# Kernel optimization log

Measured on AMD Instinct MI355X. Metric: run time of the kernel, lower is better.

The kernel has to match this reference:

```python
import jax, jax.numpy as jnp
from jax import lax
import numpy as np

C, C_MID, K_ENC, K_UP, SCALE = 128, 64, 3, 5, 2
B, H, W = 4, 48, 48
BN_EPS = 1e-3  # ultralytics Conv BN eps
EPS = 1e-6


def setup_inputs() -> dict:
    key = jax.random.key(0)
    ks = jax.random.split(key, 12)
    n_enc = (SCALE * K_UP) ** 2  # 100
    return {
        "x": jax.random.uniform(ks[0], (B, C, H, W), dtype=jnp.float32),
        "comp_w": jax.random.normal(ks[1], (C_MID, C, 1, 1), dtype=jnp.float32) * 0.05,
        "comp_bn_g": jax.random.normal(ks[2], (C_MID,), dtype=jnp.float32) * 0.1 + 1.0,
        "comp_bn_b": jax.random.normal(ks[3], (C_MID,), dtype=jnp.float32) * 0.1,
        "comp_bn_m": jax.random.normal(ks[4], (C_MID,), dtype=jnp.float32) * 0.1,
        "comp_bn_v": jax.random.uniform(ks[5], (C_MID,), dtype=jnp.float32, minval=0.5, maxval=1.5),
        "enc_w": jax.random.normal(ks[6], (n_enc, C_MID, K_ENC, K_ENC), dtype=jnp.float32) * 0.05,
        "enc_bn_g": jax.random.normal(ks[7], (n_enc,), dtype=jnp.float32) * 0.1 + 1.0,
        "enc_bn_b": jax.random.normal(ks[8], (n_enc,), dtype=jnp.float32) * 0.1,
        "enc_bn_m": jax.random.normal(ks[9], (n_enc,), dtype=jnp.float32) * 0.1,
        "enc_bn_v": jax.random.uniform(ks[10], (n_enc,), dtype=jnp.float32, minval=0.5, maxval=1.5),
    }


def _conv_bn(x, w, g, b, m, v, pad, act):
    y = lax.conv_general_dilated(
        x, w, window_strides=(1, 1), padding=[(pad, pad), (pad, pad)],
        dimension_numbers=("NCHW", "OIHW", "NCHW"))
    scale = (g * lax.rsqrt(v + BN_EPS))[None, :, None, None]
    y = (y - m[None, :, None, None]) * scale + b[None, :, None, None]
    if act:  # SiLU
        y = y * jax.nn.sigmoid(y)
    return y


def reference(x, comp_w, comp_bn_g, comp_bn_b, comp_bn_m, comp_bn_v,
              enc_w, enc_bn_g, enc_bn_b, enc_bn_m, enc_bn_v):
    b, c, h, w = x.shape
    h_, w_ = h * SCALE, w * SCALE

    # ---- SAGamma: self-adaptive gamma correction ----
    gray = 0.299 * x[:, 0] + 0.587 * x[:, 1] + 0.114 * x[:, 2]  # (b,h,w)
    gm = jnp.mean(gray, axis=(1, 2), keepdims=True)              # (b,1,1)
    gs = jnp.std(gray, axis=(1, 2), ddof=1, keepdims=True)       # unbiased, like torch
    gamma = 0.8 + (1.2 - 0.8) * gm / (gm + jnp.maximum(gs, EPS))
    gamma = jnp.clip(gamma, 0.8, 1.2)[:, None]                   # (b,1,1,1)
    x = jnp.power(x + EPS, gamma)

    # ---- CARAFE ----
    # kernel prediction: comp (1x1 Conv+BN+SiLU) -> enc (3x3 Conv+BN, no act)
    Wk = _conv_bn(x, comp_w, comp_bn_g, comp_bn_b, comp_bn_m, comp_bn_v, pad=0, act=True)
    Wk = _conv_bn(Wk, enc_w, enc_bn_g, enc_bn_b, enc_bn_m, enc_bn_v, pad=K_ENC // 2, act=False)
    # pixel shuffle: (b, 25*s*s, h, w) -> (b, 25, h_, w_)
    k2 = K_UP * K_UP
    Wk = Wk.reshape(b, k2, SCALE, SCALE, h, w)
    Wk = Wk.transpose(0, 1, 4, 2, 5, 3).reshape(b, k2, h_, w_)
    Wk = jax.nn.softmax(Wk, axis=1)

    # nearest upsample x2
    Xu = jnp.repeat(jnp.repeat(x, SCALE, axis=2), SCALE, axis=3)  # (b,c,h_,w_)
    # unfold with kernel 5, dilation 2, pad 4 -> (b,c,25,h_,w_), torch (c,kh,kw) ordering
    pad = (K_UP // 2) * SCALE
    Xp = jnp.pad(Xu, ((0, 0), (0, 0), (pad, pad), (pad, pad)))
    patches = jnp.stack(
        [Xp[:, :, i * SCALE:i * SCALE + h_, j * SCALE:j * SCALE + w_]
         for i in range(K_UP) for j in range(K_UP)], axis=2)      # (b,c,25,h_,w_)

    return jnp.einsum("bkhw,bckhw->bchw", Wk, patches)
```

## Files before the change

### kernel.cpp

```cpp
#include <hip/hip_runtime.h>
#include <hip/hip_bf16.h>
#include <math.h>

#define CB   128
#define CMID 64
#define NENC 100
#define HH   48
#define WW   48
#define BB   4
#define HW   (HH*WW)
#define H2   (HH*2)
#define W2   (WW*2)
#define PS   56
#define PROWS 50
#define PCOL0 4
#define PLANE (PROWS*PS)
#define EG   2

__global__ void halo_kernel(float* __restrict__ y1p) {
    int idx = blockIdx.x * blockDim.x + threadIdx.x;
    int plane = idx / 124;
    int t = idx % 124;
    float* p = y1p + (size_t)plane * PLANE;
    float4 z = make_float4(0.f, 0.f, 0.f, 0.f);
    if (t < 14) {
        *(float4*)(p + t * 4) = z;
    } else if (t < 28) {
        *(float4*)(p + 49 * PS + (t - 14) * 4) = z;
    } else {
        int s = t - 28;
        int r = 1 + (s >> 1);
        int col = (s & 1) ? 52 : 0;
        *(float4*)(p + r * PS + col) = z;
    }
}

__global__ void gamma_kernel(const float* __restrict__ x, float* __restrict__ gamma) {
    int b = blockIdx.x;
    const float* xb = x + (size_t)b * CB * HW;
    const float4* R4 = (const float4*)xb;
    const float4* G4 = (const float4*)(xb + HW);
    const float4* B4 = (const float4*)(xb + 2 * HW);
    float s = 0.f, s2 = 0.f;
    for (int i = threadIdx.x; i < HW / 4; i += blockDim.x) {
        float4 r = R4[i], g = G4[i], bl = B4[i];
        float g0 = 0.299f * r.x + 0.587f * g.x + 0.114f * bl.x;
        float g1 = 0.299f * r.y + 0.587f * g.y + 0.114f * bl.y;
        float g2 = 0.299f * r.z + 0.587f * g.z + 0.114f * bl.z;
        float g3 = 0.299f * r.w + 0.587f * g.w + 0.114f * bl.w;
        s  += (g0 + g1) + (g2 + g3);
        s2 += (g0 * g0 + g1 * g1) + (g2 * g2 + g3 * g3);
    }
    for (int o = 32; o > 0; o >>= 1) {
        s  += __shfl_down(s, o);
        s2 += __shfl_down(s2, o);
    }
    __shared__ float ss[4], ss2[4];
    int wid = threadIdx.x >> 6;
    if ((threadIdx.x & 63) == 0) { ss[wid] = s; ss2[wid] = s2; }
    __syncthreads();
    if (threadIdx.x == 0) {
        float S = 0.f, S2 = 0.f;
        int nw = blockDim.x >> 6;
        for (int i = 0; i < nw; i++) { S += ss[i]; S2 += ss2[i]; }
        const float N = (float)HW;
        float gm = S / N;
        float var = (S2 - S * S / N) / (N - 1.0f);
        var = fmaxf(var, 0.f);
        float gs = sqrtf(var);
        float gam = 0.8f + 0.4f * gm / (gm + fmaxf(gs, 1e-6f));
        gam = fminf(fmaxf(gam, 0.8f), 1.2f);
        gamma[b] = gam;
    }
}

__global__ void pow_kernel(const float* __restrict__ x, const float* __restrict__ gamma,
                           float* __restrict__ xg) {
    int idx = blockIdx.x * blockDim.x + threadIdx.x;
    const int total4 = BB * CB * HW / 4;
    if (idx >= total4) return;
    int b = idx / (CB * HW / 4);
    float gam = gamma[b];
    float4 xv = ((const float4*)x)[idx];
    float4 r;
    r.x = __expf(gam * __logf(xv.x + 1e-6f));
    r.y = __expf(gam * __logf(xv.y + 1e-6f));
    r.z = __expf(gam * __logf(xv.z + 1e-6f));
    r.w = __expf(gam * __logf(xv.w + 1e-6f));
    ((float4*)xg)[idx] = r;
}

__global__ void conv1_kernel(const float* __restrict__ xg, const float* __restrict__ w,
                             const float* __restrict__ g, const float* __restrict__ bta,
                             const float* __restrict__ m, const float* __restrict__ vv,
                             float* __restrict__ y1p) {
    int idx = blockIdx.x * blockDim.x + threadIdx.x;
    const int PG = HW / 4;
    const int total = BB * CMID * PG;
    if (idx >= total) return;
    int pg = idx % PG;
    int cm = (idx / PG) % CMID;
    int b  = idx / (CMID * PG);
    const float4* xb = (const float4*)(xg + (size_t)b * CB * HW) + pg;
    const float* wc = w + cm * CB;
    float4 acc = {0.f, 0.f, 0.f, 0.f};
#pragma unroll 8
    for (int c = 0; c < CB; c++) {
        float4 xv = xb[(size_t)c * PG];
        float wv = wc[c];
        acc.x = fmaf(wv, xv.x, acc.x);
        acc.y = fmaf(wv, xv.y, acc.y);
        acc.z = fmaf(wv, xv.z, acc.z);
        acc.w = fmaf(wv, xv.w, acc.w);
    }
    float sc = g[cm] * rsqrtf(vv[cm] + 1e-3f);
    float sh = bta[cm] - m[cm] * sc;
    float4 o;
    float t;
    t = acc.x * sc + sh; o.x = t / (1.f + __expf(-t));
    t = acc.y * sc + sh; o.y = t / (1.f + __expf(-t));
    t = acc.z * sc + sh; o.z = t / (1.f + __expf(-t));
    t = acc.w * sc + sh; o.w = t / (1.f + __expf(-t));
    int row = pg / 12, col = (pg % 12) * 4;
    float* dst = y1p + ((size_t)(b * CMID + cm)) * PLANE + (row + 1) * PS + (col + PCOL0);
    *(float4*)dst = o;
}

#define FMA4(A0,A1,A2,A3, wa,wb,wc, lf,mm,rt) \
    A0 = fmaf(wa, lf,   fmaf(wb, mm.x, fmaf(wc, mm.y, A0))); \
    A1 = fmaf(wa, mm.x, fmaf(wb, mm.y, fmaf(wc, mm.z, A1))); \
    A2 = fmaf(wa, mm.y, fmaf(wb, mm.z, fmaf(wc, mm.w, A2))); \
    A3 = fmaf(wa, mm.z, fmaf(wb, mm.w, fmaf(wc, rt,   A3)));

__global__ __launch_bounds__(192) void conv3_kernel(
        const float* __restrict__ y1p, const float* __restrict__ w,
        const float* __restrict__ g, const float* __restrict__ bta,
        const float* __restrict__ m, const float* __restrict__ vv,
        float* __restrict__ wk2) {
    int blk = blockIdx.x;
    int eg  = blk % (NENC / EG);
    int tmp = blk / (NENC / EG);
    int rb  = tmp % 3, b = tmp / 3;
    int e0  = eg * EG;
    int t   = threadIdx.x;
    int row = rb * 16 + t / 12;
    int c0  = (t % 12) * 4;
    const float* wb0 = w + (size_t)e0 * CMID * 9;
    const float* wb1 = wb0 + CMID * 9;
    const float* yb = y1p + (size_t)b * CMID * PLANE + row * PS + (c0 + PCOL0);

    float a00 = 0.f, a01 = 0.f, a02 = 0.f, a03 = 0.f;
    float a10 = 0.f, a11 = 0.f, a12 = 0.f, a13 = 0.f;

    float  lf0 = yb[-1];        float4 m0 = *(const float4*)yb;          float rt0 = yb[4];
    float  lf1 = yb[PS-1];      float4 m1 = *(const float4*)(yb+PS);     float rt1 = yb[PS+4];
    float  lf2 = yb[2*PS-1];    float4 m2 = *(const float4*)(yb+2*PS);   float rt2 = yb[2*PS+4];
    float u00 = wb0[0], u01 = wb0[1], u02 = wb0[2];
    float u10 = wb0[3], u11 = wb0[4], u12 = wb0[5];
    float u20 = wb0[6], u21 = wb0[7], u22 = wb0[8];
    float v00 = wb1[0], v01 = wb1[1], v02 = wb1[2];
    float v10 = wb1[3], v11 = wb1[4], v12 = wb1[5];
    float v20 = wb1[6], v21 = wb1[7], v22 = wb1[8];

    for (int cm = 0; cm < CMID - 1; ++cm) {
        const float* yn = yb + (size_t)(cm + 1) * PLANE;
        float  nlf0 = yn[-1];       float4 nm0 = *(const float4*)yn;         float nrt0 = yn[4];
        float  nlf1 = yn[PS-1];     float4 nm1 = *(const float4*)(yn+PS);    float nrt1 = yn[PS+4];
        float  nlf2 = yn[2*PS-1];   float4 nm2 = *(const float4*)(yn+2*PS);  float nrt2 = yn[2*PS+4];
        const float* wn0 = wb0 + (cm + 1) * 9;
        const float* wn1 = wb1 + (cm + 1) * 9;
        float nu00 = wn0[0], nu01 = wn0[1], nu02 = wn0[2];
        float nu10 = wn0[3], nu11 = wn0[4], nu12 = wn0[5];
        float nu20 = wn0[6], nu21 = wn0[7], nu22 = wn0[8];
        float nv00 = wn1[0], nv01 = wn1[1], nv02 = wn1[2];
        float nv10 = wn1[3], nv11 = wn1[4], nv12 = wn1[5];
        float nv20 = wn1[6], nv21 = wn1[7], nv22 = wn1[8];

        FMA4(a00,a01,a02,a03, u00,u01,u02, lf0,m0,rt0)
        FMA4(a00,a01,a02,a03, u10,u11,u12, lf1,m1,rt1)
        FMA4(a00,a01,a02,a03, u20,u21,u22, lf2,m2,rt2)
        FMA4(a10,a11,a12,a13, v00,v01,v02, lf0,m0,rt0)
        FMA4(a10,a11,a12,a13, v10,v11,v12, lf1,m1,rt1)
        FMA4(a10,a11,a12,a13, v20,v21,v22, lf2,m2,rt2)

        lf0 = nlf0; m0 = nm0; rt0 = nrt0;
        lf1 = nlf1; m1 = nm1; rt1 = nrt1;
        lf2 = nlf2; m2 = nm2; rt2 = nrt2;
        u00 = nu00; u01 = nu01; u02 = nu02;
        u10 = nu10; u11 = nu11; u12 = nu12;
        u20 = nu20; u21 = nu21; u22 = nu22;
        v00 = nv00; v01 = nv01; v02 = nv02;
        v10 = nv10; v11 = nv11; v12 = nv12;
        v20 = nv20; v21 = nv21; v22 = nv22;
    }
    FMA4(a00,a01,a02,a03, u00,u01,u02, lf0,m0,rt0)
    FMA4(a00,a01,a02,a03, u10,u11,u12, lf1,m1,rt1)
    FMA4(a00,a01,a02,a03, u20,u21,u22, lf2,m2,rt2)
    FMA4(a10,a11,a12,a13, v00,v01,v02, lf0,m0,rt0)
    FMA4(a10,a11,a12,a13, v10,v11,v12, lf1,m1,rt1)
    FMA4(a10,a11,a12,a13, v20,v21,v22, lf2,m2,rt2)

    float sc0 = g[e0] * rsqrtf(vv[e0] + 1e-3f);
    float sh0 = bta[e0] - m[e0] * sc0;
    float sc1 = g[e0+1] * rsqrtf(vv[e0+1] + 1e-3f);
    float sh1 = bta[e0+1] - m[e0+1] * sc1;
    float* op = wk2 + (size_t)(b * NENC + e0) * HW + row * WW + c0;
    float4 o0 = {a00*sc0+sh0, a01*sc0+sh0, a02*sc0+sh0, a03*sc0+sh0};
    float4 o1 = {a10*sc1+sh1, a11*sc1+sh1, a12*sc1+sh1, a13*sc1+sh1};
    *(float4*)op = o0;
    *(float4*)(op + HW) = o1;
}

__global__ void softmax_kernel(const float* __restrict__ wk2, float* __restrict__ wsm) {
    int idx = blockIdx.x * blockDim.x + threadIdx.x;
    const int total = BB * H2 * W2;
    if (idx >= total) return;
    int Wp = idx % W2, Hp = (idx / W2) % H2, b = idx / (H2 * W2);
    int h = Hp >> 1, w = Wp >> 1;
    int off = 2 * (Hp & 1) + (Wp & 1);
    const float* base = wk2 + (size_t)b * NENC * HW + (size_t)off * HW + h * WW + w;
    float vals[25];
    float mx = -1e30f;
#pragma unroll
    for (int k = 0; k < 25; k++) {
        float tv = base[(size_t)(4 * k) * HW];
        vals[k] = tv; mx = fmaxf(mx, tv);
    }
    float sum = 0.f;
#pragma unroll
    for (int k = 0; k < 25; k++) { float e2 = __expf(vals[k] - mx); vals[k] = e2; sum += e2; }
    float inv = 1.f / sum;
#pragma unroll
    for (int k = 0; k < 25; k++)
        wsm[((size_t)(b * 25 + k) * H2 + Hp) * W2 + Wp] = vals[k] * inv;
}

__global__ void gather_kernel(const float* __restrict__ xg, const float* __restrict__ wsm,
                              float* __restrict__ out) {
    int idx = blockIdx.x * blockDim.x + threadIdx.x;
    const int total = BB * CB * HW;
    if (idx >= total) return;
    int w = idx % WW;
    int h = (idx / WW) % HH;
    int c = (idx / HW) % CB;
    int b = idx / (CB * HW);
    const float* xb = xg + ((size_t)b * CB + c) * HW;
    float xv[25];
#pragma unroll
    for (int i = 0; i < 5; i++) {
        int hy = h + i - 2;
        bool hok = (hy >= 0) && (hy < HH);
#pragma unroll
        for (int j = 0; j < 5; j++) {
            int wx = w + j - 2;
            bool ok = hok && (wx >= 0) && (wx < WW);
            xv[i * 5 + j] = ok ? xb[hy * WW + wx] : 0.f;
        }
    }
    float a0 = 0.f, a1 = 0.f, a2 = 0.f, a3 = 0.f;
    const float* wb = wsm + (size_t)b * 25 * H2 * W2;
    int r0 = (2 * h) * W2 + 2 * w;
#pragma unroll
    for (int k = 0; k < 25; k++) {
        const float* wkp = wb + (size_t)k * H2 * W2;
        float2 w0 = *(const float2*)(wkp + r0);
        float2 w1 = *(const float2*)(wkp + r0 + W2);
        float xk = xv[k];
        a0 = fmaf(w0.x, xk, a0);
        a1 = fmaf(w0.y, xk, a1);
        a2 = fmaf(w1.x, xk, a2);
        a3 = fmaf(w1.y, xk, a3);
    }
    float* ob = out + (((size_t)b * CB + c) * H2 + 2 * h) * W2 + 2 * w;
    float2 s0 = {a0, a1};
    float2 s1 = {a2, a3};
    *(float2*)ob = s0;
    *(float2*)(ob + W2) = s1;
}

extern "C" void kernel_launch(void* const* d_in, const int* in_sizes, int n_in,
                              void* d_out, int out_size, void* d_ws, size_t ws_size,
                              hipStream_t stream) {
    const float* x       = (const float*)d_in[0];
    const float* comp_w  = (const float*)d_in[1];
    const float* comp_g  = (const float*)d_in[2];
    const float* comp_b  = (const float*)d_in[3];
    const float* comp_m  = (const float*)d_in[4];
    const float* comp_v  = (const float*)d_in[5];
    const float* enc_w   = (const float*)d_in[6];
    const float* enc_g   = (const float*)d_in[7];
    const float* enc_b   = (const float*)d_in[8];
    const float* enc_m   = (const float*)d_in[9];
    const float* enc_v   = (const float*)d_in[10];
    float* out = (float*)d_out;

    float* ws = (float*)d_ws;
    float* gamma = ws;
    float* xg    = ws + 64;
    float* wk2   = xg + (size_t)BB * CB * HW;
    float* y1p   = wk2 + (size_t)BB * NENC * HW;
    float* wsm   = y1p;

    halo_kernel<<<(BB * CMID * 124) / 256, 256, 0, stream>>>(y1p);
    gamma_kernel<<<BB, 256, 0, stream>>>(x, gamma);
    {
        int total4 = BB * CB * HW / 4;
        pow_kernel<<<(total4 + 255) / 256, 256, 0, stream>>>(x, gamma, xg);
    }
    {
        int total = BB * CMID * (HW / 4);
        conv1_kernel<<<(total + 255) / 256, 256, 0, stream>>>(
            xg, comp_w, comp_g, comp_b, comp_m, comp_v, y1p);
    }
    conv3_kernel<<<BB * 3 * (NENC / EG), 192, 0, stream>>>(
        y1p, enc_w, enc_g, enc_b, enc_m, enc_v, wk2);
    {
        int total = BB * H2 * W2;
        softmax_kernel<<<(total + 255) / 256, 256, 0, stream>>>(wk2, wsm);
    }
    {
        int total = BB * CB * HW;
        gather_kernel<<<(total + 255) / 256, 256, 0, stream>>>(xg, wsm, out);
    }
}
```

Before: 172.6 us.

## Fuse softmax into gather kernel with interleaved kernel-weight layout and register tiling

The conv3 kernel now writes encoder outputs in a layout where the four pixel-shuffle sub-positions of each tap are interleaved, so one float4 load picks up all four. A new fused kernel handles one input row and half its width per block. It loads those weights into shared memory, does the softmax there, and has each thread compute 12 input columns for one channel, reusing a sliding window of x values held in registers. This drops the separate softmax pass and its global round trip and cuts redundant x reads, but each block holds 128 channels with only 384 blocks, which may limit parallelism.

```diff
diff --git a/kernel.cpp b/kernel.cpp
--- a/kernel.cpp
+++ b/kernel.cpp
@@ -136,7 +136,7 @@
         const float* __restrict__ y1p, const float* __restrict__ w,
         const float* __restrict__ g, const float* __restrict__ bta,
         const float* __restrict__ m, const float* __restrict__ vv,
-        float* __restrict__ wk2) {
+        float* __restrict__ wk2n) {
     int blk = blockIdx.x;
     int eg  = blk % (NENC / EG);
     int tmp = blk / (NENC / EG);
@@ -204,78 +204,114 @@
     float sh0 = bta[e0] - m[e0] * sc0;
     float sc1 = g[e0+1] * rsqrtf(vv[e0+1] + 1e-3f);
     float sh1 = bta[e0+1] - m[e0+1] * sc1;
-    float* op = wk2 + (size_t)(b * NENC + e0) * HW + row * WW + c0;
-    float4 o0 = {a00*sc0+sh0, a01*sc0+sh0, a02*sc0+sh0, a03*sc0+sh0};
-    float4 o1 = {a10*sc1+sh1, a11*sc1+sh1, a12*sc1+sh1, a13*sc1+sh1};
-    *(float4*)op = o0;
-    *(float4*)(op + HW) = o1;
-}
-
-__global__ void softmax_kernel(const float* __restrict__ wk2, float* __restrict__ wsm) {
-    int idx = blockIdx.x * blockDim.x + threadIdx.x;
-    const int total = BB * H2 * W2;
-    if (idx >= total) return;
-    int Wp = idx % W2, Hp = (idx / W2) % H2, b = idx / (H2 * W2);
-    int h = Hp >> 1, w = Wp >> 1;
-    int off = 2 * (Hp & 1) + (Wp & 1);
-    const float* base = wk2 + (size_t)b * NENC * HW + (size_t)off * HW + h * WW + w;
-    float vals[25];
-    float mx = -1e30f;
-#pragma unroll
-    for (int k = 0; k < 25; k++) {
-        float tv = base[(size_t)(4 * k) * HW];
-        vals[k] = tv; mx = fmaxf(mx, tv);
-    }
-    float sum = 0.f;
-#pragma unroll
-    for (int k = 0; k < 25; k++) { float e2 = __expf(vals[k] - mx); vals[k] = e2; sum += e2; }
-    float inv = 1.f / sum;
-#pragma unroll
-    for (int k = 0; k < 25; k++)
-        wsm[((size_t)(b * 25 + k) * H2 + Hp) * W2 + Wp] = vals[k] * inv;
-}
-
-__global__ void gather_kernel(const float* __restrict__ xg, const float* __restrict__ wsm,
-                              float* __restrict__ out) {
-    int idx = blockIdx.x * blockDim.x + threadIdx.x;
-    const int total = BB * CB * HW;
-    if (idx >= total) return;
-    int w = idx % WW;
-    int h = (idx / WW) % HH;
-    int c = (idx / HW) % CB;
-    int b = idx / (CB * HW);
+    int kk = e0 >> 2, off0 = e0 & 3;
+    float* op = wk2n + (((size_t)(b * 25 + kk) * HW + row * WW + c0) << 2) + off0;
+    *(float2*)(op + 0)  = make_float2(a00*sc0+sh0, a10*sc1+sh1);
+    *(float2*)(op + 4)  = make_float2(a01*sc0+sh0, a11*sc1+sh1);
+    *(float2*)(op + 8)  = make_float2(a02*sc0+sh0, a12*sc1+sh1);
+    *(float2*)(op + 12) = make_float2(a03*sc0+sh0, a13*sc1+sh1);
+}
+
+__global__ __launch_bounds__(256) void sg_kernel(const float* __restrict__ xg,
+                                                 const float* __restrict__ wk2n,
+                                                 float* __restrict__ out) {
+    int blk = blockIdx.x;
+    int whalf = blk & 1;
+    int bh = blk >> 1;
+    int h = bh % HH, b = bh / HH;
+    int tid = threadIdx.x;
+
+    __shared__ float raw[25 * 24 * 4];
+    __shared__ float wsm[25 * 2 * 48];
+
+    {
+        const float4* w4p = (const float4*)wk2n;
+        size_t base4 = (size_t)b * 25 * HW + h * WW + whalf * 24;
+        float4* raw4 = (float4*)raw;
+        for (int t = tid; t < 600; t += 256) {
+            int k = t / 24, wl = t % 24;
+            raw4[t] = w4p[base4 + (size_t)k * HW + wl];
+        }
+    }
+    __syncthreads();
+    if (tid < 96) {
+        int wl = tid >> 2, off = tid & 3;
+        float v[25]; float mx = -1e30f;
+#pragma unroll
+        for (int k = 0; k < 25; k++) { v[k] = raw[(k * 24 + wl) * 4 + off]; mx = fmaxf(mx, v[k]); }
+        float sum = 0.f;
+#pragma unroll
+        for (int k = 0; k < 25; k++) { v[k] = __expf(v[k] - mx); sum += v[k]; }
+        float inv = 1.f / sum;
+        int si = off >> 1, sj = off & 1;
+#pragma unroll
+        for (int k = 0; k < 25; k++) wsm[k * 96 + si * 48 + 2 * wl + sj] = v[k] * inv;
+    }
+    __syncthreads();
+
+    int c = tid >> 1, q = tid & 1;
     const float* xb = xg + ((size_t)b * CB + c) * HW;
-    float xv[25];
+    int wbase = whalf * 24 + q * 12;
+    float* ob = out + (((size_t)b * CB + c) * H2 + 2 * h) * W2;
+    const float4* wsm4 = (const float4*)wsm;
+    const float4 Z4 = make_float4(0.f, 0.f, 0.f, 0.f);
+
+    float4 A[5], Bv[5], Cv[5];
 #pragma unroll
     for (int i = 0; i < 5; i++) {
-        int hy = h + i - 2;
-        bool hok = (hy >= 0) && (hy < HH);
-#pragma unroll
-        for (int j = 0; j < 5; j++) {
-            int wx = w + j - 2;
-            bool ok = hok && (wx >= 0) && (wx < WW);
-            xv[i * 5 + j] = ok ? xb[hy * WW + wx] : 0.f;
+        int hr = h + i - 2;
+        bool rv = (hr >= 0) && (hr < HH);
+        const float* rp = xb + hr * WW;
+        A[i]  = (rv && wbase > 0) ? *(const float4*)(rp + wbase - 4) : Z4;
+        Bv[i] = rv                ? *(const float4*)(rp + wbase)     : Z4;
+        Cv[i] = rv                ? *(const float4*)(rp + wbase + 4) : Z4;
+    }
+
+#pragma unroll
+    for (int s = 0; s < 3; s++) {
+        int wc = wbase + 4 * s;
+        float acc0[8], acc1[8];
+#pragma unroll
+        for (int p = 0; p < 8; p++) { acc0[p] = 0.f; acc1[p] = 0.f; }
+#pragma unroll
+        for (int i = 0; i < 5; i++) {
+            float xv[12] = {A[i].x, A[i].y, A[i].z, A[i].w,
+                            Bv[i].x, Bv[i].y, Bv[i].z, Bv[i].w,
+                            Cv[i].x, Cv[i].y, Cv[i].z, Cv[i].w};
+#pragma unroll
+            for (int j = 0; j < 5; j++) {
+                int k = i * 5 + j;
+                float4 w0a = wsm4[k * 24 + 6 * q + 2 * s];
+                float4 w0b = wsm4[k * 24 + 6 * q + 2 * s + 1];
+                float4 w1a = wsm4[k * 24 + 12 + 6 * q + 2 * s];
+                float4 w1b = wsm4[k * 24 + 12 + 6 * q + 2 * s + 1];
+                float x0 = xv[j + 2], x1 = xv[j + 3], x2 = xv[j + 4], x3 = xv[j + 5];
+                acc0[0] = fmaf(w0a.x, x0, acc0[0]); acc0[1] = fmaf(w0a.y, x0, acc0[1]);
+                acc0[2] = fmaf(w0a.z, x1, acc0[2]); acc0[3] = fmaf(w0a.w, x1, acc0[3]);
+                acc0[4] = fmaf(w0b.x, x2, acc0[4]); acc0[5] = fmaf(w0b.y, x2, acc0[5]);
+                acc0[6] = fmaf(w0b.z, x3, acc0[6]); acc0[7] = fmaf(w0b.w, x3, acc0[7]);
+                acc1[0] = fmaf(w1a.x, x0, acc1[0]); acc1[1] = fmaf(w1a.y, x0, acc1[1]);
+                acc1[2] = fmaf(w1a.z, x1, acc1[2]); acc1[3] = fmaf(w1a.w, x1, acc1[3]);
+                acc1[4] = fmaf(w1b.x, x2, acc1[4]); acc1[5] = fmaf(w1b.y, x2, acc1[5]);
+                acc1[6] = fmaf(w1b.z, x3, acc1[6]); acc1[7] = fmaf(w1b.w, x3, acc1[7]);
+            }
         }
-    }
-    float a0 = 0.f, a1 = 0.f, a2 = 0.f, a3 = 0.f;
-    const float* wb = wsm + (size_t)b * 25 * H2 * W2;
-    int r0 = (2 * h) * W2 + 2 * w;
-#pragma unroll
-    for (int k = 0; k < 25; k++) {
-        const float* wkp = wb + (size_t)k * H2 * W2;
-        float2 w0 = *(const float2*)(wkp + r0);
-        float2 w1 = *(const float2*)(wkp + r0 + W2);
-        float xk = xv[k];
-        a0 = fmaf(w0.x, xk, a0);
-        a1 = fmaf(w0.y, xk, a1);
-        a2 = fmaf(w1.x, xk, a2);
-        a3 = fmaf(w1.y, xk, a3);
-    }
-    float* ob = out + (((size_t)b * CB + c) * H2 + 2 * h) * W2 + 2 * w;
-    float2 s0 = {a0, a1};
-    float2 s1 = {a2, a3};
-    *(float2*)ob = s0;
-    *(float2*)(ob + W2) = s1;
+        int colg = whalf * 48 + 24 * q + 8 * s;
+        *(float4*)(ob + colg)          = make_float4(acc0[0], acc0[1], acc0[2], acc0[3]);
+        *(float4*)(ob + colg + 4)      = make_float4(acc0[4], acc0[5], acc0[6], acc0[7]);
+        *(float4*)(ob + W2 + colg)     = make_float4(acc1[0], acc1[1], acc1[2], acc1[3]);
+        *(float4*)(ob + W2 + colg + 4) = make_float4(acc1[4], acc1[5], acc1[6], acc1[7]);
+        if (s < 2) {
+            int nc = wc + 8;
+#pragma unroll
+            for (int i = 0; i < 5; i++) {
+                int hr = h + i - 2;
+                bool rv = (hr >= 0) && (hr < HH);
+                A[i] = Bv[i]; Bv[i] = Cv[i];
+                Cv[i] = (rv && nc < WW) ? *(const float4*)(xb + hr * WW + nc) : Z4;
+            }
+        }
+    }
 }
 
 extern "C" void kernel_launch(void* const* d_in, const int* in_sizes, int n_in,
@@ -297,9 +333,8 @@
     float* ws = (float*)d_ws;
     float* gamma = ws;
     float* xg    = ws + 64;
-    float* wk2   = xg + (size_t)BB * CB * HW;
-    float* y1p   = wk2 + (size_t)BB * NENC * HW;
-    float* wsm   = y1p;
+    float* wk2n  = xg + (size_t)BB * CB * HW;
+    float* y1p   = wk2n + (size_t)BB * 25 * HW * 4;
 
     halo_kernel<<<(BB * CMID * 124) / 256, 256, 0, stream>>>(y1p);
     gamma_kernel<<<BB, 256, 0, stream>>>(x, gamma);
@@ -313,13 +348,6 @@
             xg, comp_w, comp_g, comp_b, comp_m, comp_v, y1p);
     }
     conv3_kernel<<<BB * 3 * (NENC / EG), 192, 0, stream>>>(
-        y1p, enc_w, enc_g, enc_b, enc_m, enc_v, wk2);
-    {
-        int total = BB * H2 * W2;
-        softmax_kernel<<<(total + 255) / 256, 256, 0, stream>>>(wk2, wsm);
-    }
-    {
-        int total = BB * CB * HW;
-        gather_kernel<<<(total + 255) / 256, 256, 0, stream>>>(xg, wsm, out);
-    }
-}
+        y1p, enc_w, enc_g, enc_b, enc_m, enc_v, wk2n);
+    sg_kernel<<<BB * HH * 2, 256, 0, stream>>>(xg, wk2n, out);
+}
```

Measured after the change: 168.1 us. -2.6%, faster.
